# Optimization experiments

Measured on AMD Instinct MI355X. Metric: run time of the kernel, lower is better.

## Reference

```python
import jax, jax.numpy as jnp
import numpy as np

EMBED_DIM = 768
HIDDEN_DIM = 768
ASPECT_NUM = 32
BATCH = 256


def setup_inputs() -> dict:
    key = jax.random.key(0)
    k1, k2, k3, k4, k5, k6, k7 = jax.random.split(key, 7)
    s = 0.02
    return {
        "v_X": jax.random.normal(k1, (BATCH, EMBED_DIM), dtype=jnp.float32),
        "v_H": jax.random.normal(k2, (BATCH, HIDDEN_DIM), dtype=jnp.float32),
        "aspect_ids": jax.random.randint(k3, (BATCH,), 0, ASPECT_NUM, dtype=jnp.int64),
        "W1_embs": s * jax.random.normal(k4, (ASPECT_NUM, (EMBED_DIM + HIDDEN_DIM) * HIDDEN_DIM), dtype=jnp.float32),
        "b1_embs": s * jax.random.normal(k5, (ASPECT_NUM, HIDDEN_DIM), dtype=jnp.float32),
        "W2_embs": s * jax.random.normal(k6, (ASPECT_NUM, HIDDEN_DIM * 2), dtype=jnp.float32),
        "b2_embs": s * jax.random.normal(k7, (ASPECT_NUM, 2), dtype=jnp.float32),
    }


def reference(v_X, v_H, aspect_ids, W1_embs, b1_embs, W2_embs, b2_embs):
    batch = v_X.shape[0]
    V = jnp.concatenate([v_X, v_H], axis=-1)  # (B, E+H)
    W1 = W1_embs[aspect_ids].reshape(batch, EMBED_DIM + HIDDEN_DIM, HIDDEN_DIM)
    b1 = b1_embs[aspect_ids]                  # (B, H)
    W2 = W2_embs[aspect_ids].reshape(batch, HIDDEN_DIM, 2)
    b2 = b2_embs[aspect_ids]                  # (B, 2)
    out1 = jax.nn.relu(jnp.einsum('bd,bdh->bh', V, W1) + b1)  # per-sample GEMV
    logits = jnp.einsum('bh,bht->bt', out1, W2) + b2
    return logits
```

## Files before the change

kernel.cpp:

```cpp
#include <hip/hip_runtime.h>
#include <hip/hip_bf16.h>

#define EMBED 768
#define HID 768
#define DTOT 1536
#define NASP 32
#define BATCHN 256
#define CH 8
#define MAXCHUNK 64
#define NTILE 6
#define DSPLIT 8
#define DROWS (DTOT / DSPLIT)

#define META_ASPECT(c)  (1 + (c))
#define META_CNT(c)     (1 + MAXCHUNK + (c))
#define META_SMP(c, j)  (1 + 2 * MAXCHUNK + (c) * CH + (j))

__global__ __launch_bounds__(BATCHN) void bucket_kernel(
    const int* __restrict__ aspect_ids, int* __restrict__ meta)
{
    __shared__ int counts[NASP];
    __shared__ int chunkbase[NASP];
    int t = threadIdx.x;
    if (t < NASP) counts[t] = 0;
    __syncthreads();
    int a = aspect_ids[t];
    int r = atomicAdd(&counts[a], 1);
    __syncthreads();
    if (t == 0) {
        int c = 0;
        for (int i = 0; i < NASP; ++i) {
            chunkbase[i] = c;
            int n = counts[i];
            int nc = (n + CH - 1) / CH;
            for (int j = 0; j < nc; ++j) {
                meta[META_ASPECT(c + j)] = i;
                int rem = n - j * CH;
                meta[META_CNT(c + j)] = rem < CH ? rem : CH;
            }
            c += nc;
        }
        meta[0] = c;
    }
    __syncthreads();
    int c = chunkbase[a] + r / CH;
    meta[META_SMP(c, r % CH)] = t;
}

__global__ __launch_bounds__(256) void gemv1_kernel(
    const float* __restrict__ vX, const float* __restrict__ vH,
    const float* __restrict__ W1, const int* __restrict__ meta,
    float* __restrict__ part)
{
    int nchunks = meta[0];
    int bid = blockIdx.x;
    int chunk = bid / (NTILE * DSPLIT);
    if (chunk >= nchunks) return;
    int rem  = bid % (NTILE * DSPLIT);
    int tile = rem / DSPLIT;
    int dsp  = rem % DSPLIT;

    int aspect = meta[META_ASPECT(chunk)];
    int cnt    = meta[META_CNT(chunk)];

    __shared__ int smp[CH];
    __shared__ __align__(16) float Vs[DROWS][CH];
    __shared__ float4 red[256];

    int t = threadIdx.x;
    if (t < CH) {
        smp[t] = (t < cnt) ? meta[META_SMP(chunk, t)] : meta[META_SMP(chunk, 0)];
    }
    __syncthreads();

    int dbase = dsp * DROWS;
    for (int r = 0; r < 2; ++r) {
        int id = t + r * 256;
        if (id < CH * (DROWS / 4)) {
            int s = id / (DROWS / 4);
            int f = id % (DROWS / 4);
            int d = dbase + f * 4;
            const float* src = (dbase < EMBED)
                ? (vX + (size_t)smp[s] * EMBED + d)
                : (vH + (size_t)smp[s] * HID + (d - EMBED));
            float4 v = *(const float4*)src;
            Vs[f * 4 + 0][s] = v.x;
            Vs[f * 4 + 1][s] = v.y;
            Vs[f * 4 + 2][s] = v.z;
            Vs[f * 4 + 3][s] = v.w;
        }
    }
    __syncthreads();

    int c32 = t & 31;
    int dg  = t >> 5;
    int h   = tile * 128 + c32 * 4;

    const float* wp = W1 + (size_t)aspect * ((size_t)DTOT * HID)
                         + (size_t)(dbase + dg) * HID + h;

    float4 acc[CH];
    #pragma unroll
    for (int s = 0; s < CH; ++s) { acc[s].x = acc[s].y = acc[s].z = acc[s].w = 0.f; }

    #pragma unroll 4
    for (int k = 0; k < DROWS / 8; ++k) {
        float4 w = *(const float4*)wp;
        wp += 8 * HID;
        int d = k * 8 + dg;
        float4 vlo = *(const float4*)&Vs[d][0];
        float4 vhi = *(const float4*)&Vs[d][4];
        acc[0].x += vlo.x * w.x; acc[0].y += vlo.x * w.y; acc[0].z += vlo.x * w.z; acc[0].w += vlo.x * w.w;
        acc[1].x += vlo.y * w.x; acc[1].y += vlo.y * w.y; acc[1].z += vlo.y * w.z; acc[1].w += vlo.y * w.w;
        acc[2].x += vlo.z * w.x; acc[2].y += vlo.z * w.y; acc[2].z += vlo.z * w.z; acc[2].w += vlo.z * w.w;
        acc[3].x += vlo.w * w.x; acc[3].y += vlo.w * w.y; acc[3].z += vlo.w * w.z; acc[3].w += vlo.w * w.w;
        acc[4].x += vhi.x * w.x; acc[4].y += vhi.x * w.y; acc[4].z += vhi.x * w.z; acc[4].w += vhi.x * w.w;
        acc[5].x += vhi.y * w.x; acc[5].y += vhi.y * w.y; acc[5].z += vhi.y * w.z; acc[5].w += vhi.y * w.w;
        acc[6].x += vhi.z * w.x; acc[6].y += vhi.z * w.y; acc[6].z += vhi.z * w.z; acc[6].w += vhi.z * w.w;
        acc[7].x += vhi.w * w.x; acc[7].y += vhi.w * w.y; acc[7].z += vhi.w * w.z; acc[7].w += vhi.w * w.w;
    }

    size_t dsp_off = (size_t)dsp * BATCHN * HID;
    for (int s = 0; s < CH; ++s) {
        __syncthreads();
        red[t] = acc[s];
        __syncthreads();
        if (t < 32) {
            float4 sum = red[t];
            #pragma unroll
            for (int g = 1; g < 8; ++g) {
                float4 o = red[g * 32 + t];
                sum.x += o.x; sum.y += o.y; sum.z += o.z; sum.w += o.w;
            }
            *(float4*)&part[dsp_off + (size_t)smp[s] * HID + tile * 128 + t * 4] = sum;
        }
    }
}

__global__ __launch_bounds__(64) void head_kernel(
    const float* __restrict__ part, const int* __restrict__ aspect_ids,
    const float* __restrict__ b1, const float* __restrict__ W2,
    const float* __restrict__ b2, float* __restrict__ logits)
{
    int s = blockIdx.x;
    int t = threadIdx.x;
    int a = aspect_ids[s];
    const float* w2 = W2 + (size_t)a * HID * 2;
    const float* b1p = b1 + (size_t)a * HID;
    float p0 = 0.f, p1 = 0.f;
    #pragma unroll
    for (int j = 0; j < HID / 64; ++j) {
        int hh = t + j * 64;
        float o = 0.f;
        #pragma unroll
        for (int p = 0; p < DSPLIT; ++p) {
            o += part[(size_t)p * BATCHN * HID + (size_t)s * HID + hh];
        }
        o = fmaxf(o + b1p[hh], 0.f);
        p0 += o * w2[hh * 2 + 0];
        p1 += o * w2[hh * 2 + 1];
    }
    #pragma unroll
    for (int off = 32; off > 0; off >>= 1) {
        p0 += __shfl_down(p0, off, 64);
        p1 += __shfl_down(p1, off, 64);
    }
    if (t == 0) {
        logits[s * 2 + 0] = p0 + b2[a * 2 + 0];
        logits[s * 2 + 1] = p1 + b2[a * 2 + 1];
    }
}

extern "C" void kernel_launch(void* const* d_in, const int* in_sizes, int n_in,
                              void* d_out, int out_size, void* d_ws, size_t ws_size,
                              hipStream_t stream) {
    const float* vX  = (const float*)d_in[0];
    const float* vH  = (const float*)d_in[1];
    const int*   aid = (const int*)d_in[2];
    const float* W1  = (const float*)d_in[3];
    const float* b1  = (const float*)d_in[4];
    const float* W2  = (const float*)d_in[5];
    const float* b2  = (const float*)d_in[6];
    float* logits = (float*)d_out;

    int*   meta = (int*)d_ws;
    float* part = (float*)((char*)d_ws + 4096);

    bucket_kernel<<<1, BATCHN, 0, stream>>>(aid, meta);
    gemv1_kernel<<<MAXCHUNK * NTILE * DSPLIT, 256, 0, stream>>>(vX, vH, W1, meta, part);
    head_kernel<<<BATCHN, 64, 0, stream>>>(part, aid, b1, W2, b2, logits);
}
```

Before: 43.26 us.

## Fuse aspect bucketing into GEMV kernel and widen chunks to 16 samples

Drops the separate single-block bucketing kernel. Each GEMV block now recomputes the aspect grouping itself in shared memory, using wave ballots and a prefix scan. Chunk size grows from 8 to 16 samples, so each W1 tile load is reused across twice as many samples. The cap on chunks falls from 64 to 48, and the reduction now handles two samples per pass. The costs are redundant bucketing work in every block, more accumulator registers (64 floats) under a 4-blocks-per-CU launch bound, and extra shared memory. Tiny aspect groups also waste more of each 16-wide chunk.

```diff
diff --git a/kernel.cpp b/kernel.cpp
--- a/kernel.cpp
+++ b/kernel.cpp
@@ -6,89 +6,92 @@
 #define DTOT 1536
 #define NASP 32
 #define BATCHN 256
-#define CH 8
-#define MAXCHUNK 64
+#define CH 16
+#define MAXCHUNK 48
 #define NTILE 6
 #define DSPLIT 8
 #define DROWS (DTOT / DSPLIT)
 
-#define META_ASPECT(c)  (1 + (c))
-#define META_CNT(c)     (1 + MAXCHUNK + (c))
-#define META_SMP(c, j)  (1 + 2 * MAXCHUNK + (c) * CH + (j))
-
-__global__ __launch_bounds__(BATCHN) void bucket_kernel(
-    const int* __restrict__ aspect_ids, int* __restrict__ meta)
-{
-    __shared__ int counts[NASP];
-    __shared__ int chunkbase[NASP];
-    int t = threadIdx.x;
-    if (t < NASP) counts[t] = 0;
-    __syncthreads();
-    int a = aspect_ids[t];
-    int r = atomicAdd(&counts[a], 1);
-    __syncthreads();
-    if (t == 0) {
-        int c = 0;
-        for (int i = 0; i < NASP; ++i) {
-            chunkbase[i] = c;
-            int n = counts[i];
-            int nc = (n + CH - 1) / CH;
-            for (int j = 0; j < nc; ++j) {
-                meta[META_ASPECT(c + j)] = i;
-                int rem = n - j * CH;
-                meta[META_CNT(c + j)] = rem < CH ? rem : CH;
-            }
-            c += nc;
-        }
-        meta[0] = c;
-    }
-    __syncthreads();
-    int c = chunkbase[a] + r / CH;
-    meta[META_SMP(c, r % CH)] = t;
-}
-
-__global__ __launch_bounds__(256) void gemv1_kernel(
+__global__ __launch_bounds__(256, 4) void gemv1_kernel(
     const float* __restrict__ vX, const float* __restrict__ vH,
-    const float* __restrict__ W1, const int* __restrict__ meta,
+    const float* __restrict__ W1, const int* __restrict__ aspect_ids,
     float* __restrict__ part)
 {
-    int nchunks = meta[0];
+    __shared__ int wcnt[4][NASP];
+    __shared__ int basearr[NASP];
+    __shared__ int countsarr[NASP];
+    __shared__ int chasp[MAXCHUNK];
+    __shared__ int smpall[MAXCHUNK][CH];
+    __shared__ int nchunks_s;
+    __shared__ __align__(16) float Vs[DROWS][CH];
+    __shared__ __align__(16) float4 red[512];
+
+    int t = threadIdx.x;
+    int lane = t & 63;
+    int wave = t >> 6;
+    int myaid = aspect_ids[t];
+
+    unsigned long long mymask = 0ull;
+    for (int a = 0; a < NASP; ++a) {
+        bool p = (myaid == a);
+        unsigned long long m = __ballot(p);
+        if (p) mymask = m;
+        if (lane == a) wcnt[wave][a] = __popcll(m);
+    }
+    __syncthreads();
+    if (t < NASP) {
+        int ctot = wcnt[0][t] + wcnt[1][t] + wcnt[2][t] + wcnt[3][t];
+        countsarr[t] = ctot;
+        int nc = (ctot + CH - 1) / CH;
+        int incl = nc;
+        #pragma unroll
+        for (int off = 1; off < NASP; off <<= 1) {
+            int v = __shfl_up(incl, off, 64);
+            if (t >= off) incl += v;
+        }
+        int base = incl - nc;
+        basearr[t] = base;
+        for (int j = 0; j < nc; ++j) chasp[base + j] = t;
+        if (t == NASP - 1) nchunks_s = incl;
+    }
+    __syncthreads();
+    {
+        int pre = 0;
+        for (int w2 = 0; w2 < wave; ++w2) pre += wcnt[w2][myaid];
+        int r = pre + __popcll(mymask & ((1ull << lane) - 1ull));
+        int c = basearr[myaid] + r / CH;
+        smpall[c][r % CH] = t;
+    }
+    __syncthreads();
+
     int bid = blockIdx.x;
     int chunk = bid / (NTILE * DSPLIT);
-    if (chunk >= nchunks) return;
+    if (chunk >= nchunks_s) return;
     int rem  = bid % (NTILE * DSPLIT);
     int tile = rem / DSPLIT;
     int dsp  = rem % DSPLIT;
 
-    int aspect = meta[META_ASPECT(chunk)];
-    int cnt    = meta[META_CNT(chunk)];
-
-    __shared__ int smp[CH];
-    __shared__ __align__(16) float Vs[DROWS][CH];
-    __shared__ float4 red[256];
-
-    int t = threadIdx.x;
-    if (t < CH) {
-        smp[t] = (t < cnt) ? meta[META_SMP(chunk, t)] : meta[META_SMP(chunk, 0)];
-    }
-    __syncthreads();
+    int aspect = chasp[chunk];
+    int cnt = countsarr[aspect] - CH * (chunk - basearr[aspect]);
+    if (cnt > CH) cnt = CH;
 
     int dbase = dsp * DROWS;
-    for (int r = 0; r < 2; ++r) {
+
+    #pragma unroll
+    for (int r = 0; r < 3; ++r) {
         int id = t + r * 256;
-        if (id < CH * (DROWS / 4)) {
-            int s = id / (DROWS / 4);
-            int f = id % (DROWS / 4);
-            int d = dbase + f * 4;
-            const float* src = (dbase < EMBED)
-                ? (vX + (size_t)smp[s] * EMBED + d)
-                : (vH + (size_t)smp[s] * HID + (d - EMBED));
-            float4 v = *(const float4*)src;
-            Vs[f * 4 + 0][s] = v.x;
-            Vs[f * 4 + 1][s] = v.y;
-            Vs[f * 4 + 2][s] = v.z;
-            Vs[f * 4 + 3][s] = v.w;
-        }
+        int s = id & (CH - 1);
+        int f = id >> 4;
+        int smp = (s < cnt) ? smpall[chunk][s] : smpall[chunk][0];
+        int d = dbase + f * 4;
+        const float* src = (dbase < EMBED)
+            ? (vX + (size_t)smp * EMBED + d)
+            : (vH + (size_t)smp * HID + (d - EMBED));
+        float4 v = *(const float4*)src;
+        Vs[f * 4 + 0][s] = v.x;
+        Vs[f * 4 + 1][s] = v.y;
+        Vs[f * 4 + 2][s] = v.z;
+        Vs[f * 4 + 3][s] = v.w;
     }
     __syncthreads();
 
@@ -108,31 +111,49 @@
         float4 w = *(const float4*)wp;
         wp += 8 * HID;
         int d = k * 8 + dg;
-        float4 vlo = *(const float4*)&Vs[d][0];
-        float4 vhi = *(const float4*)&Vs[d][4];
-        acc[0].x += vlo.x * w.x; acc[0].y += vlo.x * w.y; acc[0].z += vlo.x * w.z; acc[0].w += vlo.x * w.w;
-        acc[1].x += vlo.y * w.x; acc[1].y += vlo.y * w.y; acc[1].z += vlo.y * w.z; acc[1].w += vlo.y * w.w;
-        acc[2].x += vlo.z * w.x; acc[2].y += vlo.z * w.y; acc[2].z += vlo.z * w.z; acc[2].w += vlo.z * w.w;
-        acc[3].x += vlo.w * w.x; acc[3].y += vlo.w * w.y; acc[3].z += vlo.w * w.z; acc[3].w += vlo.w * w.w;
-        acc[4].x += vhi.x * w.x; acc[4].y += vhi.x * w.y; acc[4].z += vhi.x * w.z; acc[4].w += vhi.x * w.w;
-        acc[5].x += vhi.y * w.x; acc[5].y += vhi.y * w.y; acc[5].z += vhi.y * w.z; acc[5].w += vhi.y * w.w;
-        acc[6].x += vhi.z * w.x; acc[6].y += vhi.z * w.y; acc[6].z += vhi.z * w.z; acc[6].w += vhi.z * w.w;
-        acc[7].x += vhi.w * w.x; acc[7].y += vhi.w * w.y; acc[7].z += vhi.w * w.z; acc[7].w += vhi.w * w.w;
+        float4 va = *(const float4*)&Vs[d][0];
+        float4 vb = *(const float4*)&Vs[d][4];
+        float4 vc = *(const float4*)&Vs[d][8];
+        float4 vd = *(const float4*)&Vs[d][12];
+        acc[0].x  += va.x * w.x; acc[0].y  += va.x * w.y; acc[0].z  += va.x * w.z; acc[0].w  += va.x * w.w;
+        acc[1].x  += va.y * w.x; acc[1].y  += va.y * w.y; acc[1].z  += va.y * w.z; acc[1].w  += va.y * w.w;
+        acc[2].x  += va.z * w.x; acc[2].y  += va.z * w.y; acc[2].z  += va.z * w.z; acc[2].w  += va.z * w.w;
+        acc[3].x  += va.w * w.x; acc[3].y  += va.w * w.y; acc[3].z  += va.w * w.z; acc[3].w  += va.w * w.w;
+        acc[4].x  += vb.x * w.x; acc[4].y  += vb.x * w.y; acc[4].z  += vb.x * w.z; acc[4].w  += vb.x * w.w;
+        acc[5].x  += vb.y * w.x; acc[5].y  += vb.y * w.y; acc[5].z  += vb.y * w.z; acc[5].w  += vb.y * w.w;
+        acc[6].x  += vb.z * w.x; acc[6].y  += vb.z * w.y; acc[6].z  += vb.z * w.z; acc[6].w  += vb.z * w.w;
+        acc[7].x  += vb.w * w.x; acc[7].y  += vb.w * w.y; acc[7].z  += vb.w * w.z; acc[7].w  += vb.w * w.w;
+        acc[8].x  += vc.x * w.x; acc[8].y  += vc.x * w.y; acc[8].z  += vc.x * w.z; acc[8].w  += vc.x * w.w;
+        acc[9].x  += vc.y * w.x; acc[9].y  += vc.y * w.y; acc[9].z  += vc.y * w.z; acc[9].w  += vc.y * w.w;
+        acc[10].x += vc.z * w.x; acc[10].y += vc.z * w.y; acc[10].z += vc.z * w.z; acc[10].w += vc.z * w.w;
+        acc[11].x += vc.w * w.x; acc[11].y += vc.w * w.y; acc[11].z += vc.w * w.z; acc[11].w += vc.w * w.w;
+        acc[12].x += vd.x * w.x; acc[12].y += vd.x * w.y; acc[12].z += vd.x * w.z; acc[12].w += vd.x * w.w;
+        acc[13].x += vd.y * w.x; acc[13].y += vd.y * w.y; acc[13].z += vd.y * w.z; acc[13].w += vd.y * w.w;
+        acc[14].x += vd.z * w.x; acc[14].y += vd.z * w.y; acc[14].z += vd.z * w.z; acc[14].w += vd.z * w.w;
+        acc[15].x += vd.w * w.x; acc[15].y += vd.w * w.y; acc[15].z += vd.w * w.z; acc[15].w += vd.w * w.w;
     }
 
     size_t dsp_off = (size_t)dsp * BATCHN * HID;
-    for (int s = 0; s < CH; ++s) {
+    #pragma unroll
+    for (int sp = 0; sp < CH / 2; ++sp) {
         __syncthreads();
-        red[t] = acc[s];
+        red[t]       = acc[2 * sp + 0];
+        red[256 + t] = acc[2 * sp + 1];
         __syncthreads();
-        if (t < 32) {
-            float4 sum = red[t];
+        if (t < 64) {
+            int half = t >> 5;
+            int l32  = t & 31;
+            int s = 2 * sp + half;
+            float4 sum = red[half * 256 + l32];
             #pragma unroll
             for (int g = 1; g < 8; ++g) {
-                float4 o = red[g * 32 + t];
+                float4 o = red[half * 256 + g * 32 + l32];
                 sum.x += o.x; sum.y += o.y; sum.z += o.z; sum.w += o.w;
             }
-            *(float4*)&part[dsp_off + (size_t)smp[s] * HID + tile * 128 + t * 4] = sum;
+            if (s < cnt) {
+                int smp = smpall[chunk][s];
+                *(float4*)&part[dsp_off + (size_t)smp * HID + tile * 128 + l32 * 4] = sum;
+            }
         }
     }
 }
@@ -183,10 +204,8 @@
     const float* b2  = (const float*)d_in[6];
     float* logits = (float*)d_out;
 
-    int*   meta = (int*)d_ws;
-    float* part = (float*)((char*)d_ws + 4096);
-
-    bucket_kernel<<<1, BATCHN, 0, stream>>>(aid, meta);
-    gemv1_kernel<<<MAXCHUNK * NTILE * DSPLIT, 256, 0, stream>>>(vX, vH, W1, meta, part);
+    float* part = (float*)d_ws;
+
+    gemv1_kernel<<<MAXCHUNK * NTILE * DSPLIT, 256, 0, stream>>>(vX, vH, W1, aid, part);
     head_kernel<<<BATCHN, 64, 0, stream>>>(part, aid, b1, W2, b2, logits);
 }
```

Result: faster. 40.09 us (-7.3%).
